# Performance work log

Hardware: AMD Instinct MI355X
Metric: run time of the kernel (lower is better)

The kernel has to match this reference:

```python
import jax, jax.numpy as jnp
import numpy as np

B, C, L = 32, 64, 4096
HIDDEN = 64
SR = 50.0
KS = (7, 15, 31, 63)
PHYS = 12
EPS_BN = 1e-5
EPS_GN = 1e-5


def _dwconv(x, w):
    # x: (B,C,L), w: (C,1,k) depthwise kernel, SAME padding for odd k
    k = w.shape[-1]
    p = (k - 1) // 2
    return jax.lax.conv_general_dilated(
        x, w, window_strides=(1,), padding=[(p, p)],
        dimension_numbers=('NCH', 'OIH', 'NCH'),
        feature_group_count=x.shape[1])


def _physics(x):
    b, c, l = x.shape
    svm = jnp.sqrt((x * x).sum(axis=1))                      # (B,L) channel norm
    svm_max = svm.max(axis=-1)
    svm_mean = svm.mean(axis=-1)
    svm_std = jnp.std(svm, axis=-1, ddof=1) + 1e-6           # torch.std is unbiased
    jerk = jnp.diff(x, axis=-1) * SR                         # (B,C,L-1)
    jerk_max = jnp.abs(jerk).max(axis=-1).mean(axis=-1)      # (B,)
    jerk_rate = jnp.diff(jerk, axis=-1) * SR
    jerk_rate_max = jnp.abs(jerk_rate).max(axis=-1).mean(axis=-1)
    sign_changes = (x[:, :, :-1] * x[:, :, 1:] < 0).astype(x.dtype)
    zcr = sign_changes.sum(axis=-1).mean(axis=-1) / l
    thr = (svm_mean + 2.0 * svm_std)[:, None]
    impact_duration = (svm > thr).astype(x.dtype).sum(axis=-1) / l
    hthr = (svm_mean + 3.0 * svm_std)[:, None]
    impact_ratio = (svm > hthr).astype(x.dtype).sum(axis=-1) / l
    free_fall = (svm < (svm_mean - svm_std)[:, None]).astype(x.dtype).sum(axis=-1) / l
    second_half = svm[:, l // 2:]
    post_stillness = jnp.tanh(1.0 / (jnp.std(second_half, axis=-1, ddof=1) + 1e-6))
    third = max(1, l // 3)
    pre_mean = svm[:, :third].mean(axis=-1)
    impact_peak = svm[:, third:2 * third].max(axis=-1)
    post_mean = svm[:, 2 * third:].mean(axis=-1)
    fall_phase = jax.nn.relu(impact_peak - pre_mean) + jax.nn.relu(impact_peak - post_mean)
    fall_phase = fall_phase / (jnp.abs(impact_peak) + 1e-6)
    spectrum = jnp.fft.rfft(x.astype(jnp.float32), axis=-1, norm='ortho')
    power = (jnp.abs(spectrum) ** 2).sum(axis=1)             # (B, L//2+1)
    freqs = jnp.linspace(0.0, 1.0, power.shape[-1], dtype=power.dtype)
    total_power = power.sum(axis=-1) + 1e-6
    spectral_centroid = (power * freqs).sum(axis=-1) / total_power
    high_freq_ratio = jnp.where(freqs > 0.4, power, 0.0).sum(axis=-1) / total_power
    feats = jnp.stack([svm_max, svm_mean, jerk_max, jerk_rate_max, zcr,
                       impact_duration, impact_ratio, post_stillness, free_fall,
                       spectral_centroid, high_freq_ratio, fall_phase], axis=-1)
    return jnp.nan_to_num(feats, nan=0.0, posinf=0.0, neginf=0.0).astype(x.dtype)


def _forward(x, dw_w7, dw_w15, dw_w31, dw_w63, bn_g, bn_b, bn_m, bn_v,
             comp_w1, comp_b1, comp_w2, comp_b2,
             pn_g, pn_b, pn_m, pn_v,
             pe_w1, pe_b1, pe_w2, pe_b2, pg_w, pg_b,
             temperature, gn_g, gn_b, proj_w, proj_b, res_scale):
    # 4 depthwise conv + BN(eval) branches
    branches = []
    for i, w in enumerate((dw_w7, dw_w15, dw_w31, dw_w63)):
        y = _dwconv(x, w)
        y = (y - bn_m[i][None, :, None]) / jnp.sqrt(bn_v[i][None, :, None] + EPS_BN) \
            * bn_g[i][None, :, None] + bn_b[i][None, :, None]
        branches.append(y)
    stacked = jnp.stack(branches, axis=1)                    # (B,4,C,L)
    # complexity net: global avg pool -> MLP
    xm = x.mean(axis=-1)                                     # (B,C)
    h = jax.nn.relu(xm @ comp_w1 + comp_b1)
    complexity_logits = h @ comp_w2 + comp_b2                # (B,4)
    # physics gate
    pf = _physics(x)                                         # (B,12)
    pf = (pf - pn_m) / jnp.sqrt(pn_v + EPS_BN) * pn_g + pn_b
    pe = jax.nn.relu(jax.nn.relu(pf @ pe_w1 + pe_b1) @ pe_w2 + pe_b2)
    physics_weights = jax.nn.sigmoid(pe @ pg_w + pg_b)       # (B,4)
    temp = jnp.maximum(temperature, 0.1)
    weights = jax.nn.softmax(complexity_logits * physics_weights / temp, axis=-1)
    mixed = jnp.einsum('bkcl,bk->bcl', stacked, weights)
    # proj: GroupNorm(1,C) -> GELU(exact) -> 1x1 conv
    mu = mixed.mean(axis=(1, 2), keepdims=True)
    var = mixed.var(axis=(1, 2), keepdims=True)
    gn = (mixed - mu) / jnp.sqrt(var + EPS_GN) * gn_g[None, :, None] + gn_b[None, :, None]
    act = jax.nn.gelu(gn, approximate=False)
    out = jnp.einsum('oc,bcl->bol', proj_w, act) + proj_b[None, :, None]
    return x + res_scale * out


def setup_inputs() -> dict:
    ks = jax.random.split(jax.random.key(0), 16)
    f32 = jnp.float32
    inp = {}
    inp['x'] = jax.random.normal(ks[0], (B, C, L), dtype=f32)
    for i, k in enumerate(KS):
        inp[f'dw_w{k}'] = jax.random.normal(ks[1 + i], (C, 1, k), dtype=f32) / np.sqrt(k)
    inp['bn_g'] = jnp.ones((4, C), f32)
    inp['bn_b'] = jnp.zeros((4, C), f32)
    inp['bn_m'] = 0.1 * jax.random.normal(ks[5], (4, C), dtype=f32)
    inp['bn_v'] = jax.random.uniform(ks[6], (4, C), dtype=f32, minval=0.5, maxval=1.5)
    inp['comp_w1'] = jax.random.normal(ks[7], (C, HIDDEN), dtype=f32) / np.sqrt(C)
    inp['comp_b1'] = jnp.zeros((HIDDEN,), f32)
    inp['comp_w2'] = jax.random.normal(ks[8], (HIDDEN, 4), dtype=f32) / np.sqrt(HIDDEN)
    inp['comp_b2'] = jnp.zeros((4,), f32)
    inp['pn_g'] = jnp.ones((PHYS,), f32)
    inp['pn_b'] = jnp.zeros((PHYS,), f32)
    inp['pn_m'] = 0.1 * jax.random.normal(ks[9], (PHYS,), dtype=f32)
    inp['pn_v'] = jax.random.uniform(ks[10], (PHYS,), dtype=f32, minval=0.5, maxval=1.5)
    inp['pe_w1'] = jax.random.normal(ks[11], (PHYS, 32), dtype=f32) / np.sqrt(PHYS)
    inp['pe_b1'] = jnp.zeros((32,), f32)
    inp['pe_w2'] = jax.random.normal(ks[12], (32, 32), dtype=f32) / np.sqrt(32)
    inp['pe_b2'] = jnp.zeros((32,), f32)
    inp['pg_w'] = jax.random.normal(ks[13], (32, 4), dtype=f32) / np.sqrt(32)
    inp['pg_b'] = jnp.zeros((4,), f32)
    inp['temperature'] = jnp.asarray(1.0, f32)
    inp['gn_g'] = jnp.ones((C,), f32)
    inp['gn_b'] = jnp.zeros((C,), f32)
    inp['proj_w'] = jax.random.normal(ks[14], (C, C), dtype=f32) / np.sqrt(C)
    inp['proj_b'] = jnp.zeros((C,), f32)
    inp['res_scale'] = jnp.asarray(0.5, f32)  # init is 0.0; 0.5 gives a non-trivial output
    return inp


def reference(x, dw_w7, dw_w15, dw_w31, dw_w63, bn_g, bn_b, bn_m, bn_v,
              comp_w1, comp_b1, comp_w2, comp_b2,
              pn_g, pn_b, pn_m, pn_v,
              pe_w1, pe_b1, pe_w2, pe_b2, pg_w, pg_b,
              temperature, gn_g, gn_b, proj_w, proj_b, res_scale):
    return _forward(x, dw_w7, dw_w15, dw_w31, dw_w63, bn_g, bn_b, bn_m, bn_v,
                    comp_w1, comp_b1, comp_w2, comp_b2, pn_g, pn_b, pn_m, pn_v,
                    pe_w1, pe_b1, pe_w2, pe_b2, pg_w, pg_b,
                    temperature, gn_g, gn_b, proj_w, proj_b, res_scale)
```

## Files before the change

### kernel.cpp

```cpp
#include <hip/hip_runtime.h>
#include <math.h>

#define LN 4096
#define CN 64
#define BQ 32
#define NTH 256

#define OFF_CHAN_SUM    0
#define OFF_CHAN_JERK   2048
#define OFF_CHAN_JRATE  4096
#define OFF_CHAN_ZCR    6144
#define OFF_SVMST_PART  8192
#define OFF_SPEC_PART   12288
#define OFF_EFF_B       15360
#define OFF_GNP         17408
#define OFF_EFF_W       21504
#define OFF_SVMBUF      152576

#define FP(i) ((i) + ((i) >> 4))

__device__ __forceinline__ void bfly4(float2& a, float2& b, float2& c, float2& d,
                                      float w1r, float w1i, float w2r, float w2i,
                                      float w3r, float w3i) {
  float t1r = b.x*w1r - b.y*w1i, t1i = b.x*w1i + b.y*w1r;
  float t2r = c.x*w2r - c.y*w2i, t2i = c.x*w2i + c.y*w2r;
  float t3r = d.x*w3r - d.y*w3i, t3i = d.x*w3i + d.y*w3r;
  float ar = a.x + t2r, ai = a.y + t2i;
  float br = a.x - t2r, bi = a.y - t2i;
  float cr = t1r + t3r, ci = t1i + t3i;
  float dr = t1r - t3r, di = t1i - t3i;
  a = make_float2(ar + cr, ai + ci);
  b = make_float2(br + di, bi - dr);
  c = make_float2(ar - cr, ai - ci);
  d = make_float2(br - di, bi + dr);
}

__global__ __launch_bounds__(NTH) void kS(const float* __restrict__ x, float* __restrict__ ws) {
  __shared__ __align__(16) char smraw[34880];
  int role = blockIdx.x;
  int t = threadIdx.x;

  if (role < 2048) {
    int bc = role;
    const float* row = x + (size_t)bc * LN;
    int l0 = t * 16;
    float rd[18];
    const float4* r4 = (const float4*)(row + l0);
#pragma unroll
    for (int q = 0; q < 4; q++) {
      float4 v = r4[q];
      rd[4*q] = v.x; rd[4*q+1] = v.y; rd[4*q+2] = v.z; rd[4*q+3] = v.w;
    }
    if (t < 255) { rd[16] = row[l0 + 16]; rd[17] = row[l0 + 17]; }
    else { rd[16] = 0.f; rd[17] = 0.f; }
    float lsum = 0.f, jm = 0.f, jrm = 0.f; int zc = 0;
#pragma unroll
    for (int i = 0; i < 16; i++) {
      float a = rd[i], b2 = rd[i+1];
      lsum += a;
      int l = l0 + i;
      if (l < LN - 1) {
        jm = fmaxf(jm, fabsf(b2 - a));
        zc += (a * b2 < 0.f);
        if (l < LN - 2) jrm = fmaxf(jrm, fabsf(rd[i+2] - 2.f*b2 + a));
      }
    }
    for (int off = 32; off > 0; off >>= 1) {
      lsum += __shfl_down(lsum, off);
      jm = fmaxf(jm, __shfl_down(jm, off));
      jrm = fmaxf(jrm, __shfl_down(jrm, off));
      zc += __shfl_down(zc, off);
    }
    float* s1 = (float*)smraw; float* s2_ = s1 + 4; float* s3 = s1 + 8; int* s4 = (int*)(s1 + 12);
    int w = t >> 6;
    if ((t & 63) == 0) { s1[w] = lsum; s2_[w] = jm; s3[w] = jrm; s4[w] = zc; }
    __syncthreads();
    if (t == 0) {
      float S = 0, J = 0, JR = 0; int Z = 0;
      for (int i = 0; i < 4; i++) { S += s1[i]; J = fmaxf(J, s2_[i]); JR = fmaxf(JR, s3[i]); Z += s4[i]; }
      ws[OFF_CHAN_SUM + bc]   = S;
      ws[OFF_CHAN_JERK + bc]  = J * 50.f;
      ws[OFF_CHAN_JRATE + bc] = JR * 2500.f;
      ws[OFF_CHAN_ZCR + bc]   = (float)Z;
    }
  } else if (role < 2560) {
    int blk = role - 2048;
    int b = blk >> 4, lt = blk & 15;
    int l = lt * 256 + t;
    const float* xb = x + (size_t)b * CN * LN + l;
    float acc = 0.f;
#pragma unroll
    for (int c = 0; c < CN; c++) { float v = xb[(size_t)c * LN]; acc = fmaf(v, v, acc); }
    float svm = sqrtf(acc);
    ws[OFF_SVMBUF + (size_t)b * LN + l] = svm;
    const int third = LN / 3;
    float vS = svm, vS2 = svm * svm;
    float vS2H  = (l >= LN/2) ? svm : 0.f;
    float vS2H2 = (l >= LN/2) ? svm * svm : 0.f;
    float vPRE  = (l < third) ? svm : 0.f;
    float vPOST = (l >= 2*third) ? svm : 0.f;
    float vMX = svm;
    float vMID = (l >= third && l < 2*third) ? svm : 0.f;
    for (int off = 32; off > 0; off >>= 1) {
      vS += __shfl_down(vS, off); vS2 += __shfl_down(vS2, off);
      vS2H += __shfl_down(vS2H, off); vS2H2 += __shfl_down(vS2H2, off);
      vPRE += __shfl_down(vPRE, off); vPOST += __shfl_down(vPOST, off);
      vMX = fmaxf(vMX, __shfl_down(vMX, off));
      vMID = fmaxf(vMID, __shfl_down(vMID, off));
    }
    float (*red)[4] = (float(*)[4])smraw;
    int w = t >> 6;
    if ((t & 63) == 0) {
      red[0][w] = vS; red[1][w] = vS2; red[2][w] = vMX; red[3][w] = vS2H;
      red[4][w] = vS2H2; red[5][w] = vPRE; red[6][w] = vMID; red[7][w] = vPOST;
    }
    __syncthreads();
    if (t == 0) {
      float* sp = ws + OFF_SVMST_PART + (size_t)blk * 8;
      sp[0] = red[0][0]+red[0][1]+red[0][2]+red[0][3];
      sp[1] = red[1][0]+red[1][1]+red[1][2]+red[1][3];
      sp[2] = fmaxf(fmaxf(red[2][0],red[2][1]),fmaxf(red[2][2],red[2][3]));
      sp[3] = red[3][0]+red[3][1]+red[3][2]+red[3][3];
      sp[4] = red[4][0]+red[4][1]+red[4][2]+red[4][3];
      sp[5] = red[5][0]+red[5][1]+red[5][2]+red[5][3];
      sp[6] = fmaxf(fmaxf(red[6][0],red[6][1]),fmaxf(red[6][2],red[6][3]));
      sp[7] = red[7][0]+red[7][1]+red[7][2]+red[7][3];
    }
  } else {
    int blk = role - 2560;
    int b = blk >> 5, cp = blk & 31;
    const float* r0 = x + ((size_t)b * CN + 2 * cp) * LN;
    const float* r1 = r0 + LN;
    float2* z = (float2*)smraw;
    float (*red)[4] = (float(*)[4])(smraw + 34816);
#pragma unroll
    for (int k = 0; k < 4; k++) {
      int n4 = (k * 256 + t) * 4;
      float4 a = *(const float4*)(r0 + n4);
      float4 c = *(const float4*)(r1 + n4);
      float ar[4] = {a.x, a.y, a.z, a.w}, cr[4] = {c.x, c.y, c.z, c.w};
#pragma unroll
      for (int q = 0; q < 4; q++) {
        unsigned n = (unsigned)(n4 + q);
        unsigned br = __brev(n) >> 20;
        unsigned dr = ((br & 0x555u) << 1) | ((br & 0xAAAu) >> 1);
        z[FP(dr)] = make_float2(ar[q], cr[q]);
      }
    }
    __syncthreads();
    const float c8r[4] = { 1.f, 0.92387953251f, 0.70710678119f, 0.38268343236f };
    const float c8i[4] = { 0.f, -0.38268343236f, -0.70710678119f, -0.92387953251f };
#pragma unroll
    for (int p = 0; p < 3; p++) {
      const int H = (p == 0) ? 1 : (p == 1) ? 16 : 256;
      int r = t & (H - 1);
      int B = ((t / H) * 16 * H) + r;
      float2 E[16];
#pragma unroll
      for (int q = 0; q < 16; q++) E[q] = z[FP(B + q * H)];
      float su, cu;
      sincospif((float)r / (8.0f * (float)H), &su, &cu);
      float ur = cu, ui = -su;
      float u2r = ur*ur - ui*ui, u2i = 2.f*ur*ui;
      float w1r = u2r*u2r - u2i*u2i, w1i = 2.f*u2r*u2i;
      float w2r = w1r*w1r - w1i*w1i, w2i = 2.f*w1r*w1i;
      float w3r = w2r*w1r - w2i*w1i, w3i = w2r*w1i + w2i*w1r;
#pragma unroll
      for (int m = 0; m < 4; m++)
        bfly4(E[4*m], E[4*m+1], E[4*m+2], E[4*m+3], w1r, w1i, w2r, w2i, w3r, w3i);
#pragma unroll
      for (int m = 0; m < 4; m++) {
        float W1r = ur*c8r[m] - ui*c8i[m];
        float W1i = ur*c8i[m] + ui*c8r[m];
        float W2r = W1r*W1r - W1i*W1i, W2i = 2.f*W1r*W1i;
        float W3r = W2r*W1r - W2i*W1i, W3i = W2r*W1i + W2i*W1r;
        bfly4(E[m], E[m+4], E[m+8], E[m+12], W1r, W1i, W2r, W2i, W3r, W3i);
      }
#pragma unroll
      for (int q = 0; q < 16; q++) z[FP(B + q * H)] = E[q];
      __syncthreads();
    }
    float tot = 0.f, cen = 0.f, hi = 0.f;
    for (int k = t; k <= LN / 2; k += NTH) {
      float p;
      if (k == 0 || k == LN / 2) {
        float2 v = z[FP(k)];
        p = v.x * v.x + v.y * v.y;
      } else {
        float2 zk = z[FP(k)], zn = z[FP(LN - k)];
        float a1 = zk.x + zn.x, a2 = zk.y - zn.y, a3 = zk.y + zn.y, a4 = zk.x - zn.x;
        p = 0.25f * (a1*a1 + a2*a2 + a3*a3 + a4*a4);
      }
      p *= (1.0f / LN);
      tot += p;
      cen += p * ((float)k * (1.0f / (LN / 2)));
      if (k >= 820) hi += p;
    }
    for (int off = 32; off > 0; off >>= 1) {
      tot += __shfl_down(tot, off);
      cen += __shfl_down(cen, off);
      hi  += __shfl_down(hi, off);
    }
    int w = t >> 6;
    if ((t & 63) == 0) { red[0][w] = tot; red[1][w] = cen; red[2][w] = hi; }
    __syncthreads();
    if (t == 0) {
      float* sp = ws + OFF_SPEC_PART + (size_t)blk * 3;
      sp[0] = red[0][0]+red[0][1]+red[0][2]+red[0][3];
      sp[1] = red[1][0]+red[1][1]+red[1][2]+red[1][3];
      sp[2] = red[2][0]+red[2][1]+red[2][2]+red[2][3];
    }
  }
}

__global__ __launch_bounds__(NTH) void k4_gate(
    const float* __restrict__ dw7, const float* __restrict__ dw15,
    const float* __restrict__ dw31, const float* __restrict__ dw63,
    const float* __restrict__ bn_g, const float* __restrict__ bn_b,
    const float* __restrict__ bn_m, const float* __restrict__ bn_v,
    const float* __restrict__ comp_w1, const float* __restrict__ comp_b1,
    const float* __restrict__ comp_w2, const float* __restrict__ comp_b2,
    const float* __restrict__ pn_g, const float* __restrict__ pn_b,
    const float* __restrict__ pn_m, const float* __restrict__ pn_v,
    const float* __restrict__ pe_w1, const float* __restrict__ pe_b1,
    const float* __restrict__ pe_w2, const float* __restrict__ pe_b2,
    const float* __restrict__ pg_w, const float* __restrict__ pg_b,
    const float* __restrict__ temperature,
    float* __restrict__ ws)
{
  int b = blockIdx.x, t = threadIdx.x;
  __shared__ float sp8[16][8];
  __shared__ float sp3[32][3];
  __shared__ float stv[10];
  __shared__ float bc2[2];
  __shared__ float xm[64], h[64], pf[12], pe1v[32], pe2v[32], lgts[4], wts[4];
  __shared__ int ri[3][4], cnts[3];
  if (t < 16) {
    const float* p = ws + OFF_SVMST_PART + (size_t)(b * 16 + t) * 8;
#pragma unroll
    for (int i = 0; i < 8; i++) sp8[t][i] = p[i];
  }
  if (t >= 32 && t < 64) {
    int i = t - 32;
    const float* p = ws + OFF_SPEC_PART + (size_t)(b * 32 + i) * 3;
    sp3[i][0] = p[0]; sp3[i][1] = p[1]; sp3[i][2] = p[2];
  }
  __syncthreads();
  if (t == 0) {
    float S=0,S2=0,MX=-1e30f,S2H=0,S2H2=0,PRE=0,MID=-1e30f,POST=0;
    for (int i = 0; i < 16; i++) {
      S += sp8[i][0]; S2 += sp8[i][1]; MX = fmaxf(MX, sp8[i][2]);
      S2H += sp8[i][3]; S2H2 += sp8[i][4]; PRE += sp8[i][5];
      MID = fmaxf(MID, sp8[i][6]); POST += sp8[i][7];
    }
    float tot=0,cen=0,hi=0;
    for (int i = 0; i < 32; i++) { tot += sp3[i][0]; cen += sp3[i][1]; hi += sp3[i][2]; }
    stv[0]=S; stv[1]=S2; stv[2]=MX; stv[3]=S2H; stv[4]=S2H2;
    stv[5]=PRE; stv[6]=MID; stv[7]=POST; stv[8]=cen/(tot+1e-6f); stv[9]=hi/(tot+1e-6f);
    float mean = S * (1.f / LN);
    float var = (S2 - S * S * (1.f / LN)) * (1.f / (LN - 1));
    var = fmaxf(var, 0.f);
    bc2[0] = mean;
    bc2[1] = sqrtf(var) + 1e-6f;
  }
  __syncthreads();
  float mean = bc2[0], stde = bc2[1];
  float thr2 = mean + 2.f * stde, thr3 = mean + 3.f * stde, thrf = mean - stde;
  const float* svm = ws + OFF_SVMBUF + (size_t)b * LN;
  int c2 = 0, c3 = 0, cf = 0;
  for (int l = t; l < LN; l += NTH) {
    float v = svm[l];
    c2 += (v > thr2); c3 += (v > thr3); cf += (v < thrf);
  }
  for (int off = 32; off > 0; off >>= 1) {
    c2 += __shfl_down(c2, off); c3 += __shfl_down(c3, off); cf += __shfl_down(cf, off);
  }
  int w = t >> 6;
  if ((t & 63) == 0) { ri[0][w] = c2; ri[1][w] = c3; ri[2][w] = cf; }
  float j = 0.f, jr = 0.f, zz = 0.f;
  if (t < 64) {
    xm[t] = ws[OFF_CHAN_SUM + b * 64 + t] * (1.0f / LN);
    j  = ws[OFF_CHAN_JERK + b * 64 + t];
    jr = ws[OFF_CHAN_JRATE + b * 64 + t];
    zz = ws[OFF_CHAN_ZCR + b * 64 + t];
    for (int off = 32; off > 0; off >>= 1) {
      j += __shfl_down(j, off); jr += __shfl_down(jr, off); zz += __shfl_down(zz, off);
    }
  }
  __syncthreads();
  if (t == 0) {
    cnts[0] = ri[0][0]+ri[0][1]+ri[0][2]+ri[0][3];
    cnts[1] = ri[1][0]+ri[1][1]+ri[1][2]+ri[1][3];
    cnts[2] = ri[2][0]+ri[2][1]+ri[2][2]+ri[2][3];
    const int third = LN / 3;
    float S2H = stv[3], S2H2 = stv[4];
    float n2 = (float)(LN / 2);
    float var2 = (S2H2 - S2H * S2H / n2) / (n2 - 1.f);
    var2 = fmaxf(var2, 0.f);
    float post_still = tanhf(1.f / (sqrtf(var2) + 1e-6f));
    float pre_mean = stv[5] / (float)third;
    float post_mean = stv[7] / (float)(LN - 2 * third);
    float pk = stv[6];
    float fp = fmaxf(pk - pre_mean, 0.f) + fmaxf(pk - post_mean, 0.f);
    fp = fp / (fabsf(pk) + 1e-6f);
    pf[0] = stv[2];
    pf[1] = mean;
    pf[2] = j * (1.f / 64);
    pf[3] = jr * (1.f / 64);
    pf[4] = (zz * (1.f / 64)) * (1.f / LN);
    pf[5] = (float)cnts[0] / LN;
    pf[6] = (float)cnts[1] / LN;
    pf[7] = post_still;
    pf[8] = (float)cnts[2] / LN;
    pf[9] = stv[8];
    pf[10] = stv[9];
    pf[11] = fp;
  }
  __syncthreads();
  if (t < 12) pf[t] = (pf[t] - pn_m[t]) * rsqrtf(pn_v[t] + 1e-5f) * pn_g[t] + pn_b[t];
  __syncthreads();
  if (t < 64) {
    float hv = comp_b1[t];
    for (int i = 0; i < 64; i++) hv = fmaf(xm[i], comp_w1[i * 64 + t], hv);
    h[t] = fmaxf(hv, 0.f);
  }
  if (t < 32) {
    float v = pe_b1[t];
    for (int i = 0; i < 12; i++) v = fmaf(pf[i], pe_w1[i * 32 + t], v);
    pe1v[t] = fmaxf(v, 0.f);
  }
  __syncthreads();
  if (t < 32) {
    float v = pe_b2[t];
    for (int i = 0; i < 32; i++) v = fmaf(pe1v[i], pe_w2[i * 32 + t], v);
    pe2v[t] = fmaxf(v, 0.f);
  }
  __syncthreads();
  if (t < 4) {
    float v = comp_b2[t];
    for (int i = 0; i < 64; i++) v = fmaf(h[i], comp_w2[i * 4 + t], v);
    float g = pg_b[t];
    for (int i = 0; i < 32; i++) g = fmaf(pe2v[i], pg_w[i * 4 + t], g);
    g = 1.f / (1.f + expf(-g));
    float temp = fmaxf(temperature[0], 0.1f);
    lgts[t] = v * g / temp;
  }
  __syncthreads();
  if (t < 4) {
    float m = fmaxf(fmaxf(lgts[0], lgts[1]), fmaxf(lgts[2], lgts[3]));
    float den = expf(lgts[0]-m) + expf(lgts[1]-m) + expf(lgts[2]-m) + expf(lgts[3]-m);
    wts[t] = expf(lgts[t] - m) / den;
  }
  __syncthreads();
  if (t < 64) {
    int c = t;
    float w0 = wts[0], w1 = wts[1], w2 = wts[2], w3 = wts[3];
    float sc0 = bn_g[0*64+c] * rsqrtf(bn_v[0*64+c] + 1e-5f);
    float sc1 = bn_g[1*64+c] * rsqrtf(bn_v[1*64+c] + 1e-5f);
    float sc2 = bn_g[2*64+c] * rsqrtf(bn_v[2*64+c] + 1e-5f);
    float sc3 = bn_g[3*64+c] * rsqrtf(bn_v[3*64+c] + 1e-5f);
    float o0 = bn_b[0*64+c] - bn_m[0*64+c] * sc0;
    float o1 = bn_b[1*64+c] - bn_m[1*64+c] * sc1;
    float o2 = bn_b[2*64+c] - bn_m[2*64+c] * sc2;
    float o3 = bn_b[3*64+c] - bn_m[3*64+c] * sc3;
    ws[OFF_EFF_B + b * 64 + c] = w0*o0 + w1*o1 + w2*o2 + w3*o3;
    float a0 = w0*sc0, a1 = w1*sc1, a2 = w2*sc2, a3 = w3*sc3;
    float* eff = ws + OFF_EFF_W + (size_t)(b * 64 + c) * 64;
    for (int tau = 0; tau < 64; tau++) {
      float v = 0.f;
      if (tau < 63) {
        v = a3 * dw63[c * 63 + tau];
        int i7 = tau - 28;  if (i7 >= 0 && i7 < 7)   v = fmaf(a0, dw7[c * 7 + i7], v);
        int i15 = tau - 24; if (i15 >= 0 && i15 < 15) v = fmaf(a1, dw15[c * 15 + i15], v);
        int i31 = tau - 16; if (i31 >= 0 && i31 < 31) v = fmaf(a2, dw31[c * 31 + i31], v);
      }
      eff[tau] = v;
    }
  }
}

__device__ __forceinline__ float4 ldmask(const float* __restrict__ row, int idx) {
  int idxc = idx < 0 ? 0 : (idx > LN - 4 ? LN - 4 : idx);
  float4 v = *(const float4*)(row + idxc);
  float m = (idx == idxc) ? 1.f : 0.f;
  v.x *= m; v.y *= m; v.z *= m; v.w *= m;
  return v;
}

#define F16(wv,a0,a1,a2,a3,a4,a5,a6,a7,a8,a9,aA,aB,aC,aD,aE,aF) \
  acc[0]=fmaf(wv,a0,acc[0]);  acc[1]=fmaf(wv,a1,acc[1]);  acc[2]=fmaf(wv,a2,acc[2]);  acc[3]=fmaf(wv,a3,acc[3]);  \
  acc[4]=fmaf(wv,a4,acc[4]);  acc[5]=fmaf(wv,a5,acc[5]);  acc[6]=fmaf(wv,a6,acc[6]);  acc[7]=fmaf(wv,a7,acc[7]);  \
  acc[8]=fmaf(wv,a8,acc[8]);  acc[9]=fmaf(wv,a9,acc[9]);  acc[10]=fmaf(wv,aA,acc[10]); acc[11]=fmaf(wv,aB,acc[11]); \
  acc[12]=fmaf(wv,aC,acc[12]); acc[13]=fmaf(wv,aD,acc[13]); acc[14]=fmaf(wv,aE,acc[14]); acc[15]=fmaf(wv,aF,acc[15]);

__global__ __launch_bounds__(NTH) void k5_conv(const float* __restrict__ x,
                                               float* __restrict__ ws,
                                               float* __restrict__ mixed_out) {
  int bc = blockIdx.x;
  int t = threadIdx.x;
  __shared__ float wt[64];
  __shared__ float biasS;
  __shared__ double rda[2][4];
  if (t < 64) wt[t] = ws[OFF_EFF_W + (size_t)bc * 64 + t];
  if (t == 0) biasS = ws[OFF_EFF_B + bc];
  const float* row = x + (size_t)bc * LN;
  int l0 = t * 16;
  int g0 = l0 - 32;
  float4 R0 = ldmask(row, g0);
  float4 R1 = ldmask(row, g0 + 4);
  float4 R2 = ldmask(row, g0 + 8);
  float4 R3 = ldmask(row, g0 + 12);
  float4 R4 = ldmask(row, g0 + 16);
  __syncthreads();
  float bias = biasS;
  float acc[16];
#pragma unroll
  for (int jj = 0; jj < 16; jj++) acc[jj] = bias;
#pragma unroll
  for (int g = 0; g < 16; g++) {
    float w0 = wt[4*g], w1 = wt[4*g+1], w2 = wt[4*g+2], w3 = wt[4*g+3];
    F16(w0, R0.y,R0.z,R0.w,R1.x,R1.y,R1.z,R1.w,R2.x,R2.y,R2.z,R2.w,R3.x,R3.y,R3.z,R3.w,R4.x)
    F16(w1, R0.z,R0.w,R1.x,R1.y,R1.z,R1.w,R2.x,R2.y,R2.z,R2.w,R3.x,R3.y,R3.z,R3.w,R4.x,R4.y)
    F16(w2, R0.w,R1.x,R1.y,R1.z,R1.w,R2.x,R2.y,R2.z,R2.w,R3.x,R3.y,R3.z,R3.w,R4.x,R4.y,R4.z)
    F16(w3, R1.x,R1.y,R1.z,R1.w,R2.x,R2.y,R2.z,R2.w,R3.x,R3.y,R3.z,R3.w,R4.x,R4.y,R4.z,R4.w)
    if (g < 15) {
      R0 = R1; R1 = R2; R2 = R3; R3 = R4;
      R4 = ldmask(row, g0 + 4 * (g + 5));
    }
  }
  double ls = 0, ls2 = 0;
#pragma unroll
  for (int jj = 0; jj < 16; jj++) { float v = acc[jj]; ls += v; ls2 += (double)v * (double)v; }
  for (int off = 32; off > 0; off >>= 1) {
    ls += __shfl_down(ls, off);
    ls2 += __shfl_down(ls2, off);
  }
  int w = t >> 6;
  if ((t & 63) == 0) { rda[0][w] = ls; rda[1][w] = ls2; }
  __syncthreads();
  if (t == 0) {
    double* gp = (double*)(ws + OFF_GNP);
    gp[2 * bc + 0] = rda[0][0]+rda[0][1]+rda[0][2]+rda[0][3];
    gp[2 * bc + 1] = rda[1][0]+rda[1][1]+rda[1][2]+rda[1][3];
  }
  float* dst = mixed_out + (size_t)bc * LN + l0;
#pragma unroll
  for (int q = 0; q < 4; q++) {
    float4 v; v.x = acc[4*q]; v.y = acc[4*q+1]; v.z = acc[4*q+2]; v.w = acc[4*q+3];
    *(float4*)(dst + 4 * q) = v;
  }
}

__global__ __launch_bounds__(NTH) void k6_final(const float* __restrict__ x,
    const float* __restrict__ proj_w, const float* __restrict__ proj_b,
    const float* __restrict__ gn_g, const float* __restrict__ gn_b,
    const float* __restrict__ res_scale,
    const float* __restrict__ ws, float* out) {
  int blk = blockIdx.x;
  int b = blk >> 5;
  int l0 = (blk & 31) * 128;
  __shared__ float actS[64 * 128];
  __shared__ float Wt[64 * 64];
  __shared__ double rg[2][4];
  __shared__ float bcst[2];
  int t = threadIdx.x;
  {
    const double* gp = (const double*)(ws + OFF_GNP) + (size_t)b * CN * 2;
    double s1 = 0, s2 = 0;
    for (int i = t; i < CN; i += NTH) { s1 += gp[2*i]; s2 += gp[2*i+1]; }
    for (int off = 32; off > 0; off >>= 1) { s1 += __shfl_down(s1, off); s2 += __shfl_down(s2, off); }
    int w = t >> 6;
    if ((t & 63) == 0) { rg[0][w] = s1; rg[1][w] = s2; }
    __syncthreads();
    if (t == 0) {
      double S1 = rg[0][0]+rg[0][1]+rg[0][2]+rg[0][3];
      double S2 = rg[1][0]+rg[1][1]+rg[1][2]+rg[1][3];
      const double NN = 64.0 * 4096.0;
      double mud = S1 / NN;
      bcst[0] = (float)mud;
      bcst[1] = rsqrtf((float)(S2 / NN - mud * mud) + 1e-5f);
    }
  }
  for (int i = t; i < 4096; i += NTH) {
    int o = i & 63, c = i >> 6;
    Wt[c * 64 + o] = proj_w[o * 64 + c];
  }
  __syncthreads();
  float mu = bcst[0], rstd = bcst[1];
  const float* mx = out + (size_t)b * CN * LN;
  for (int i = t; i < 8192; i += NTH) {
    int c = i >> 7, l = i & 127;
    float v = mx[(size_t)c * LN + l0 + l];
    float g = (v - mu) * rstd * gn_g[c] + gn_b[c];
    float a = 0.5f * g * (1.f + erff(g * 0.70710678118654752f));
    actS[c * 128 + l] = a;
  }
  __syncthreads();
  int lg = t & 31;
  int og = (t >> 5) * 8;
  float4 acc4[8];
#pragma unroll
  for (int q = 0; q < 8; q++) { acc4[q].x = 0.f; acc4[q].y = 0.f; acc4[q].z = 0.f; acc4[q].w = 0.f; }
  for (int c = 0; c < 64; c++) {
    float4 a = *(const float4*)&actS[c * 128 + lg * 4];
    float4 wlo = *(const float4*)&Wt[c * 64 + og];
    float4 whi = *(const float4*)&Wt[c * 64 + og + 4];
    float wv[8] = { wlo.x, wlo.y, wlo.z, wlo.w, whi.x, whi.y, whi.z, whi.w };
#pragma unroll
    for (int q = 0; q < 8; q++) {
      acc4[q].x = fmaf(wv[q], a.x, acc4[q].x);
      acc4[q].y = fmaf(wv[q], a.y, acc4[q].y);
      acc4[q].z = fmaf(wv[q], a.z, acc4[q].z);
      acc4[q].w = fmaf(wv[q], a.w, acc4[q].w);
    }
  }
  float rsv = res_scale[0];
  const float* xb = x + (size_t)b * CN * LN;
  float* ob = out + (size_t)b * CN * LN;
#pragma unroll
  for (int q = 0; q < 8; q++) {
    int o = og + q;
    float pb = proj_b[o];
    size_t base = (size_t)o * LN + l0 + lg * 4;
    float4 xv = *(const float4*)&xb[base];
    float4 r;
    r.x = xv.x + rsv * (acc4[q].x + pb);
    r.y = xv.y + rsv * (acc4[q].y + pb);
    r.z = xv.z + rsv * (acc4[q].z + pb);
    r.w = xv.w + rsv * (acc4[q].w + pb);
    *(float4*)&ob[base] = r;
  }
}

extern "C" void kernel_launch(void* const* d_in, const int* in_sizes, int n_in,
                              void* d_out, int out_size, void* d_ws, size_t ws_size,
                              hipStream_t stream) {
  const float* x        = (const float*)d_in[0];
  const float* dw7      = (const float*)d_in[1];
  const float* dw15     = (const float*)d_in[2];
  const float* dw31     = (const float*)d_in[3];
  const float* dw63     = (const float*)d_in[4];
  const float* bn_g     = (const float*)d_in[5];
  const float* bn_b     = (const float*)d_in[6];
  const float* bn_m     = (const float*)d_in[7];
  const float* bn_v     = (const float*)d_in[8];
  const float* comp_w1  = (const float*)d_in[9];
  const float* comp_b1  = (const float*)d_in[10];
  const float* comp_w2  = (const float*)d_in[11];
  const float* comp_b2  = (const float*)d_in[12];
  const float* pn_g     = (const float*)d_in[13];
  const float* pn_b     = (const float*)d_in[14];
  const float* pn_m     = (const float*)d_in[15];
  const float* pn_v     = (const float*)d_in[16];
  const float* pe_w1    = (const float*)d_in[17];
  const float* pe_b1    = (const float*)d_in[18];
  const float* pe_w2    = (const float*)d_in[19];
  const float* pe_b2    = (const float*)d_in[20];
  const float* pg_w     = (const float*)d_in[21];
  const float* pg_b     = (const float*)d_in[22];
  const float* temperature = (const float*)d_in[23];
  const float* gn_g     = (const float*)d_in[24];
  const float* gn_b     = (const float*)d_in[25];
  const float* proj_w   = (const float*)d_in[26];
  const float* proj_b   = (const float*)d_in[27];
  const float* res_scale= (const float*)d_in[28];
  float* ws = (float*)d_ws;
  float* out = (float*)d_out;

  hipLaunchKernelGGL(kS, dim3(2048 + 512 + 1024), dim3(NTH), 0, stream, x, ws);
  hipLaunchKernelGGL(k4_gate, dim3(BQ), dim3(NTH), 0, stream,
                     dw7, dw15, dw31, dw63, bn_g, bn_b, bn_m, bn_v,
                     comp_w1, comp_b1, comp_w2, comp_b2,
                     pn_g, pn_b, pn_m, pn_v, pe_w1, pe_b1, pe_w2, pe_b2,
                     pg_w, pg_b, temperature, ws);
  hipLaunchKernelGGL(k5_conv, dim3(BQ * CN), dim3(NTH), 0, stream, x, ws, out);
  hipLaunchKernelGGL(k6_final, dim3(BQ * 32), dim3(NTH), 0, stream,
                     x, proj_w, proj_b, gn_g, gn_b, res_scale, ws, out);
}
```

Baseline: 235.0 us.

## Fuse stats passes into FFT blocks and merge gate computation into conv kernel

The per-channel jerk/zero-crossing stats and the SVM partial sums are folded into the FFT blocks, so one 1024-block kernel reads x once for all three instead of running separate role groups. The per-batch gate kernel is merged into the depthwise conv kernel, with each block recomputing the gate redundantly, which drops a launch and the effective-weight workspace round-trip. The final projection kernel is retiled to process two 64-column halves with smaller shared memory, aiming for higher occupancy. The cost is duplicated gate arithmetic in every conv block and more work per FFT block.

New measurement: 228.7 us. -2.7%, faster.

```diff
diff --git a/kernel.cpp b/kernel.cpp
--- a/kernel.cpp
+++ b/kernel.cpp
@@ -3,7 +3,6 @@
 
 #define LN 4096
 #define CN 64
-#define BQ 32
 #define NTH 256
 
 #define OFF_CHAN_SUM    0
@@ -11,11 +10,9 @@
 #define OFF_CHAN_JRATE  4096
 #define OFF_CHAN_ZCR    6144
 #define OFF_SVMST_PART  8192
-#define OFF_SPEC_PART   12288
-#define OFF_EFF_B       15360
-#define OFF_GNP         17408
-#define OFF_EFF_W       21504
-#define OFF_SVMBUF      152576
+#define OFF_SPEC_PART   16384
+#define OFF_GNP         19584
+#define OFF_SVMBUF      27776
 
 #define FP(i) ((i) + ((i) >> 4))
 
@@ -35,131 +32,164 @@
   d = make_float2(br - di, bi + dr);
 }
 
-__global__ __launch_bounds__(NTH) void kS(const float* __restrict__ x, float* __restrict__ ws) {
-  __shared__ __align__(16) char smraw[34880];
-  int role = blockIdx.x;
+__device__ __forceinline__ float4 ldmask(const float* __restrict__ row, int idx) {
+  int idxc = idx < 0 ? 0 : (idx > LN - 4 ? LN - 4 : idx);
+  float4 v = *(const float4*)(row + idxc);
+  float m = (idx == idxc) ? 1.f : 0.f;
+  v.x *= m; v.y *= m; v.z *= m; v.w *= m;
+  return v;
+}
+
+#define F16(wv,a0,a1,a2,a3,a4,a5,a6,a7,a8,a9,aA,aB,aC,aD,aE,aF) \
+  acc[0]=fmaf(wv,a0,acc[0]);  acc[1]=fmaf(wv,a1,acc[1]);  acc[2]=fmaf(wv,a2,acc[2]);  acc[3]=fmaf(wv,a3,acc[3]);  \
+  acc[4]=fmaf(wv,a4,acc[4]);  acc[5]=fmaf(wv,a5,acc[5]);  acc[6]=fmaf(wv,a6,acc[6]);  acc[7]=fmaf(wv,a7,acc[7]);  \
+  acc[8]=fmaf(wv,a8,acc[8]);  acc[9]=fmaf(wv,a9,acc[9]);  acc[10]=fmaf(wv,aA,acc[10]); acc[11]=fmaf(wv,aB,acc[11]); \
+  acc[12]=fmaf(wv,aC,acc[12]); acc[13]=fmaf(wv,aD,acc[13]); acc[14]=fmaf(wv,aE,acc[14]); acc[15]=fmaf(wv,aF,acc[15]);
+
+__global__ __launch_bounds__(NTH) void k1_spec(const float* __restrict__ x, float* __restrict__ ws) {
+  __shared__ __align__(16) char smraw[35072];
+  int i = blockIdx.x;
+  int b = i >> 5, sl = i & 31;
   int t = threadIdx.x;
 
-  if (role < 2048) {
-    int bc = role;
-    const float* row = x + (size_t)bc * LN;
-    int l0 = t * 16;
-    float rd[18];
-    const float4* r4 = (const float4*)(row + l0);
-#pragma unroll
-    for (int q = 0; q < 4; q++) {
-      float4 v = r4[q];
-      rd[4*q] = v.x; rd[4*q+1] = v.y; rd[4*q+2] = v.z; rd[4*q+3] = v.w;
-    }
-    if (t < 255) { rd[16] = row[l0 + 16]; rd[17] = row[l0 + 17]; }
-    else { rd[16] = 0.f; rd[17] = 0.f; }
-    float lsum = 0.f, jm = 0.f, jrm = 0.f; int zc = 0;
-#pragma unroll
-    for (int i = 0; i < 16; i++) {
-      float a = rd[i], b2 = rd[i+1];
-      lsum += a;
-      int l = l0 + i;
-      if (l < LN - 1) {
-        jm = fmaxf(jm, fabsf(b2 - a));
-        zc += (a * b2 < 0.f);
-        if (l < LN - 2) jrm = fmaxf(jrm, fabsf(rd[i+2] - 2.f*b2 + a));
-      }
-    }
-    for (int off = 32; off > 0; off >>= 1) {
-      lsum += __shfl_down(lsum, off);
-      jm = fmaxf(jm, __shfl_down(jm, off));
-      jrm = fmaxf(jrm, __shfl_down(jrm, off));
-      zc += __shfl_down(zc, off);
-    }
-    float* s1 = (float*)smraw; float* s2_ = s1 + 4; float* s3 = s1 + 8; int* s4 = (int*)(s1 + 12);
-    int w = t >> 6;
-    if ((t & 63) == 0) { s1[w] = lsum; s2_[w] = jm; s3[w] = jrm; s4[w] = zc; }
-    __syncthreads();
-    if (t == 0) {
-      float S = 0, J = 0, JR = 0; int Z = 0;
-      for (int i = 0; i < 4; i++) { S += s1[i]; J = fmaxf(J, s2_[i]); JR = fmaxf(JR, s3[i]); Z += s4[i]; }
-      ws[OFF_CHAN_SUM + bc]   = S;
-      ws[OFF_CHAN_JERK + bc]  = J * 50.f;
-      ws[OFF_CHAN_JRATE + bc] = JR * 2500.f;
-      ws[OFF_CHAN_ZCR + bc]   = (float)Z;
-    }
-  } else if (role < 2560) {
-    int blk = role - 2048;
-    int b = blk >> 4, lt = blk & 15;
-    int l = lt * 256 + t;
+  {
+    float* tmp = (float*)smraw;
+    float (*sred)[8] = (float(*)[8])(smraw + 512);
+    int lt = t & 127, ch = t >> 7;
+    int l = sl * 128 + lt;
     const float* xb = x + (size_t)b * CN * LN + l;
     float acc = 0.f;
 #pragma unroll
-    for (int c = 0; c < CN; c++) { float v = xb[(size_t)c * LN]; acc = fmaf(v, v, acc); }
-    float svm = sqrtf(acc);
-    ws[OFF_SVMBUF + (size_t)b * LN + l] = svm;
-    const int third = LN / 3;
-    float vS = svm, vS2 = svm * svm;
-    float vS2H  = (l >= LN/2) ? svm : 0.f;
-    float vS2H2 = (l >= LN/2) ? svm * svm : 0.f;
-    float vPRE  = (l < third) ? svm : 0.f;
-    float vPOST = (l >= 2*third) ? svm : 0.f;
-    float vMX = svm;
-    float vMID = (l >= third && l < 2*third) ? svm : 0.f;
-    for (int off = 32; off > 0; off >>= 1) {
-      vS += __shfl_down(vS, off); vS2 += __shfl_down(vS2, off);
-      vS2H += __shfl_down(vS2H, off); vS2H2 += __shfl_down(vS2H2, off);
-      vPRE += __shfl_down(vPRE, off); vPOST += __shfl_down(vPOST, off);
-      vMX = fmaxf(vMX, __shfl_down(vMX, off));
-      vMID = fmaxf(vMID, __shfl_down(vMID, off));
-    }
-    float (*red)[4] = (float(*)[4])smraw;
-    int w = t >> 6;
-    if ((t & 63) == 0) {
-      red[0][w] = vS; red[1][w] = vS2; red[2][w] = vMX; red[3][w] = vS2H;
-      red[4][w] = vS2H2; red[5][w] = vPRE; red[6][w] = vMID; red[7][w] = vPOST;
+    for (int cc = 0; cc < 32; cc++) {
+      float v = xb[(size_t)(ch * 32 + cc) * LN];
+      acc = fmaf(v, v, acc);
+    }
+    if (ch == 1) tmp[lt] = acc;
+    __syncthreads();
+    if (ch == 0) {
+      acc += tmp[lt];
+      float svm = sqrtf(acc);
+      ws[OFF_SVMBUF + (size_t)b * LN + l] = svm;
+      const int third = LN / 3;
+      float vS = svm, vS2 = svm * svm;
+      float vS2H  = (l >= LN/2) ? svm : 0.f;
+      float vS2H2 = (l >= LN/2) ? svm * svm : 0.f;
+      float vPRE  = (l < third) ? svm : 0.f;
+      float vPOST = (l >= 2*third) ? svm : 0.f;
+      float vMX = svm;
+      float vMID = (l >= third && l < 2*third) ? svm : 0.f;
+      for (int off = 32; off > 0; off >>= 1) {
+        vS += __shfl_down(vS, off); vS2 += __shfl_down(vS2, off);
+        vS2H += __shfl_down(vS2H, off); vS2H2 += __shfl_down(vS2H2, off);
+        vPRE += __shfl_down(vPRE, off); vPOST += __shfl_down(vPOST, off);
+        vMX = fmaxf(vMX, __shfl_down(vMX, off));
+        vMID = fmaxf(vMID, __shfl_down(vMID, off));
+      }
+      if ((t & 63) == 0) {
+        int w = t >> 6;
+        sred[w][0]=vS; sred[w][1]=vS2; sred[w][2]=vMX; sred[w][3]=vS2H;
+        sred[w][4]=vS2H2; sred[w][5]=vPRE; sred[w][6]=vMID; sred[w][7]=vPOST;
+      }
     }
     __syncthreads();
     if (t == 0) {
-      float* sp = ws + OFF_SVMST_PART + (size_t)blk * 8;
-      sp[0] = red[0][0]+red[0][1]+red[0][2]+red[0][3];
-      sp[1] = red[1][0]+red[1][1]+red[1][2]+red[1][3];
-      sp[2] = fmaxf(fmaxf(red[2][0],red[2][1]),fmaxf(red[2][2],red[2][3]));
-      sp[3] = red[3][0]+red[3][1]+red[3][2]+red[3][3];
-      sp[4] = red[4][0]+red[4][1]+red[4][2]+red[4][3];
-      sp[5] = red[5][0]+red[5][1]+red[5][2]+red[5][3];
-      sp[6] = fmaxf(fmaxf(red[6][0],red[6][1]),fmaxf(red[6][2],red[6][3]));
-      sp[7] = red[7][0]+red[7][1]+red[7][2]+red[7][3];
-    }
-  } else {
-    int blk = role - 2560;
-    int b = blk >> 5, cp = blk & 31;
-    const float* r0 = x + ((size_t)b * CN + 2 * cp) * LN;
+      float* sp = ws + OFF_SVMST_PART + (size_t)(b * 32 + sl) * 8;
+      sp[0]=sred[0][0]+sred[1][0];
+      sp[1]=sred[0][1]+sred[1][1];
+      sp[2]=fmaxf(sred[0][2],sred[1][2]);
+      sp[3]=sred[0][3]+sred[1][3];
+      sp[4]=sred[0][4]+sred[1][4];
+      sp[5]=sred[0][5]+sred[1][5];
+      sp[6]=fmaxf(sred[0][6],sred[1][6]);
+      sp[7]=sred[0][7]+sred[1][7];
+    }
+    __syncthreads();
+  }
+
+  {
+    const float* r0 = x + ((size_t)b * CN + 2 * sl) * LN;
     const float* r1 = r0 + LN;
     float2* z = (float2*)smraw;
-    float (*red)[4] = (float(*)[4])(smraw + 34816);
+    float (*sred8)[8] = (float(*)[8])(smraw + 34816);
+    float s0 = 0.f, jm0 = 0.f, jr0 = 0.f; int zc0 = 0;
+    float s1v = 0.f, jm1 = 0.f, jr1 = 0.f; int zc1 = 0;
 #pragma unroll
     for (int k = 0; k < 4; k++) {
       int n4 = (k * 256 + t) * 4;
       float4 a = *(const float4*)(r0 + n4);
       float4 c = *(const float4*)(r1 + n4);
-      float ar[4] = {a.x, a.y, a.z, a.w}, cr[4] = {c.x, c.y, c.z, c.w};
+      float a4 = __shfl_down(a.x, 1), a5 = __shfl_down(a.y, 1);
+      float c4 = __shfl_down(c.x, 1), c5 = __shfl_down(c.y, 1);
+      if ((t & 63) == 63) {
+        a4 = (n4 + 4 < LN) ? r0[n4 + 4] : 0.f;
+        a5 = (n4 + 5 < LN) ? r0[n4 + 5] : 0.f;
+        c4 = (n4 + 4 < LN) ? r1[n4 + 4] : 0.f;
+        c5 = (n4 + 5 < LN) ? r1[n4 + 5] : 0.f;
+      }
+      bool nl = (n4 + 4 < LN);
+      s0 += a.x + a.y + a.z + a.w;
+      jm0 = fmaxf(jm0, fmaxf(fmaxf(fabsf(a.y-a.x), fabsf(a.z-a.y)), fabsf(a.w-a.z)));
+      zc0 += (a.x*a.y < 0.f) + (a.y*a.z < 0.f) + (a.z*a.w < 0.f);
+      jr0 = fmaxf(jr0, fmaxf(fabsf(a.z - 2.f*a.y + a.x), fabsf(a.w - 2.f*a.z + a.y)));
+      if (nl) {
+        jm0 = fmaxf(jm0, fabsf(a4 - a.w));
+        zc0 += (a.w * a4 < 0.f);
+        jr0 = fmaxf(jr0, fmaxf(fabsf(a4 - 2.f*a.w + a.z), fabsf(a5 - 2.f*a4 + a.w)));
+      }
+      s1v += c.x + c.y + c.z + c.w;
+      jm1 = fmaxf(jm1, fmaxf(fmaxf(fabsf(c.y-c.x), fabsf(c.z-c.y)), fabsf(c.w-c.z)));
+      zc1 += (c.x*c.y < 0.f) + (c.y*c.z < 0.f) + (c.z*c.w < 0.f);
+      jr1 = fmaxf(jr1, fmaxf(fabsf(c.z - 2.f*c.y + c.x), fabsf(c.w - 2.f*c.z + c.y)));
+      if (nl) {
+        jm1 = fmaxf(jm1, fabsf(c4 - c.w));
+        zc1 += (c.w * c4 < 0.f);
+        jr1 = fmaxf(jr1, fmaxf(fabsf(c4 - 2.f*c.w + c.z), fabsf(c5 - 2.f*c4 + c.w)));
+      }
+      float ar[4] = {a.x, a.y, a.z, a.w}, crr[4] = {c.x, c.y, c.z, c.w};
 #pragma unroll
       for (int q = 0; q < 4; q++) {
         unsigned n = (unsigned)(n4 + q);
         unsigned br = __brev(n) >> 20;
         unsigned dr = ((br & 0x555u) << 1) | ((br & 0xAAAu) >> 1);
-        z[FP(dr)] = make_float2(ar[q], cr[q]);
-      }
-    }
-    __syncthreads();
+        z[FP(dr)] = make_float2(ar[q], crr[q]);
+      }
+    }
+    for (int off = 32; off > 0; off >>= 1) {
+      s0 += __shfl_down(s0, off); jm0 = fmaxf(jm0, __shfl_down(jm0, off));
+      jr0 = fmaxf(jr0, __shfl_down(jr0, off)); zc0 += __shfl_down(zc0, off);
+      s1v += __shfl_down(s1v, off); jm1 = fmaxf(jm1, __shfl_down(jm1, off));
+      jr1 = fmaxf(jr1, __shfl_down(jr1, off)); zc1 += __shfl_down(zc1, off);
+    }
+    if ((t & 63) == 0) {
+      int w = t >> 6;
+      sred8[w][0]=s0; sred8[w][1]=jm0; sred8[w][2]=jr0; sred8[w][3]=(float)zc0;
+      sred8[w][4]=s1v; sred8[w][5]=jm1; sred8[w][6]=jr1; sred8[w][7]=(float)zc1;
+    }
+    __syncthreads();
+    if (t == 0) {
+      int bc0 = b * CN + 2 * sl;
+      float S0=0,J0=0,JR0=0,Z0=0,S1=0,J1=0,JR1=0,Z1=0;
+      for (int w = 0; w < 4; w++) {
+        S0 += sred8[w][0]; J0 = fmaxf(J0, sred8[w][1]); JR0 = fmaxf(JR0, sred8[w][2]); Z0 += sred8[w][3];
+        S1 += sred8[w][4]; J1 = fmaxf(J1, sred8[w][5]); JR1 = fmaxf(JR1, sred8[w][6]); Z1 += sred8[w][7];
+      }
+      ws[OFF_CHAN_SUM + bc0]       = S0;           ws[OFF_CHAN_SUM + bc0 + 1]   = S1;
+      ws[OFF_CHAN_JERK + bc0]      = J0 * 50.f;    ws[OFF_CHAN_JERK + bc0 + 1]  = J1 * 50.f;
+      ws[OFF_CHAN_JRATE + bc0]     = JR0 * 2500.f; ws[OFF_CHAN_JRATE + bc0 + 1] = JR1 * 2500.f;
+      ws[OFF_CHAN_ZCR + bc0]       = Z0;           ws[OFF_CHAN_ZCR + bc0 + 1]   = Z1;
+    }
     const float c8r[4] = { 1.f, 0.92387953251f, 0.70710678119f, 0.38268343236f };
     const float c8i[4] = { 0.f, -0.38268343236f, -0.70710678119f, -0.92387953251f };
 #pragma unroll
     for (int p = 0; p < 3; p++) {
       const int H = (p == 0) ? 1 : (p == 1) ? 16 : 256;
-      int r = t & (H - 1);
-      int B = ((t / H) * 16 * H) + r;
+      int rr = t & (H - 1);
+      int B = ((t / H) * 16 * H) + rr;
       float2 E[16];
 #pragma unroll
       for (int q = 0; q < 16; q++) E[q] = z[FP(B + q * H)];
       float su, cu;
-      sincospif((float)r / (8.0f * (float)H), &su, &cu);
+      sincospif((float)rr / (8.0f * (float)H), &su, &cu);
       float ur = cu, ui = -su;
       float u2r = ur*ur - ui*ui, u2i = 2.f*ur*ui;
       float w1r = u2r*u2r - u2i*u2i, w1i = 2.f*u2r*u2i;
@@ -188,8 +218,8 @@
         p = v.x * v.x + v.y * v.y;
       } else {
         float2 zk = z[FP(k)], zn = z[FP(LN - k)];
-        float a1 = zk.x + zn.x, a2 = zk.y - zn.y, a3 = zk.y + zn.y, a4 = zk.x - zn.x;
-        p = 0.25f * (a1*a1 + a2*a2 + a3*a3 + a4*a4);
+        float a1 = zk.x + zn.x, a2 = zk.y - zn.y, a3 = zk.y + zn.y, a4v = zk.x - zn.x;
+        p = 0.25f * (a1*a1 + a2*a2 + a3*a3 + a4v*a4v);
       }
       p *= (1.0f / LN);
       tot += p;
@@ -201,19 +231,20 @@
       cen += __shfl_down(cen, off);
       hi  += __shfl_down(hi, off);
     }
-    int w = t >> 6;
-    if ((t & 63) == 0) { red[0][w] = tot; red[1][w] = cen; red[2][w] = hi; }
+    float (*redS)[4] = (float(*)[4])(smraw + 34816);
+    if ((t & 63) == 0) { int w = t >> 6; redS[0][w] = tot; redS[1][w] = cen; redS[2][w] = hi; }
     __syncthreads();
     if (t == 0) {
-      float* sp = ws + OFF_SPEC_PART + (size_t)blk * 3;
-      sp[0] = red[0][0]+red[0][1]+red[0][2]+red[0][3];
-      sp[1] = red[1][0]+red[1][1]+red[1][2]+red[1][3];
-      sp[2] = red[2][0]+red[2][1]+red[2][2]+red[2][3];
+      float* sp = ws + OFF_SPEC_PART + (size_t)(b * 32 + sl) * 3;
+      sp[0] = redS[0][0]+redS[0][1]+redS[0][2]+redS[0][3];
+      sp[1] = redS[1][0]+redS[1][1]+redS[1][2]+redS[1][3];
+      sp[2] = redS[2][0]+redS[2][1]+redS[2][2]+redS[2][3];
     }
   }
 }
 
-__global__ __launch_bounds__(NTH) void k4_gate(
+__global__ __launch_bounds__(NTH) void k2_conv(
+    const float* __restrict__ x,
     const float* __restrict__ dw7, const float* __restrict__ dw15,
     const float* __restrict__ dw31, const float* __restrict__ dw63,
     const float* __restrict__ bn_g, const float* __restrict__ bn_b,
@@ -226,37 +257,43 @@
     const float* __restrict__ pe_w2, const float* __restrict__ pe_b2,
     const float* __restrict__ pg_w, const float* __restrict__ pg_b,
     const float* __restrict__ temperature,
-    float* __restrict__ ws)
+    float* __restrict__ ws, float* __restrict__ out)
 {
-  int b = blockIdx.x, t = threadIdx.x;
-  __shared__ float sp8[16][8];
+  int i = blockIdx.x;
+  int b = i >> 5, sl = i & 31;
+  int t = threadIdx.x;
+  __shared__ float sp8[32][8];
   __shared__ float sp3[32][3];
   __shared__ float stv[10];
   __shared__ float bc2[2];
-  __shared__ float xm[64], h[64], pf[12], pe1v[32], pe2v[32], lgts[4], wts[4];
+  __shared__ float xm[64], h[64], pf[12], pe1v[32], pe2v[32], lgts[4], swts[4];
   __shared__ int ri[3][4], cnts[3];
-  if (t < 16) {
-    const float* p = ws + OFF_SVMST_PART + (size_t)(b * 16 + t) * 8;
-#pragma unroll
-    for (int i = 0; i < 8; i++) sp8[t][i] = p[i];
+  __shared__ float cwt[2][64];
+  __shared__ float cbias[2];
+  __shared__ double rda[2][4];
+
+  if (t < 32) {
+    const float* p = ws + OFF_SVMST_PART + (size_t)(b * 32 + t) * 8;
+#pragma unroll
+    for (int q = 0; q < 8; q++) sp8[t][q] = p[q];
   }
   if (t >= 32 && t < 64) {
-    int i = t - 32;
-    const float* p = ws + OFF_SPEC_PART + (size_t)(b * 32 + i) * 3;
-    sp3[i][0] = p[0]; sp3[i][1] = p[1]; sp3[i][2] = p[2];
+    int q = t - 32;
+    const float* p = ws + OFF_SPEC_PART + (size_t)(b * 32 + q) * 3;
+    sp3[q][0] = p[0]; sp3[q][1] = p[1]; sp3[q][2] = p[2];
   }
   __syncthreads();
   if (t == 0) {
     float S=0,S2=0,MX=-1e30f,S2H=0,S2H2=0,PRE=0,MID=-1e30f,POST=0;
-    for (int i = 0; i < 16; i++) {
-      S += sp8[i][0]; S2 += sp8[i][1]; MX = fmaxf(MX, sp8[i][2]);
-      S2H += sp8[i][3]; S2H2 += sp8[i][4]; PRE += sp8[i][5];
-      MID = fmaxf(MID, sp8[i][6]); POST += sp8[i][7];
-    }
-    float tot=0,cen=0,hi=0;
-    for (int i = 0; i < 32; i++) { tot += sp3[i][0]; cen += sp3[i][1]; hi += sp3[i][2]; }
+    for (int q = 0; q < 32; q++) {
+      S += sp8[q][0]; S2 += sp8[q][1]; MX = fmaxf(MX, sp8[q][2]);
+      S2H += sp8[q][3]; S2H2 += sp8[q][4]; PRE += sp8[q][5];
+      MID = fmaxf(MID, sp8[q][6]); POST += sp8[q][7];
+    }
+    float tt=0,ce=0,hh=0;
+    for (int q = 0; q < 32; q++) { tt += sp3[q][0]; ce += sp3[q][1]; hh += sp3[q][2]; }
     stv[0]=S; stv[1]=S2; stv[2]=MX; stv[3]=S2H; stv[4]=S2H2;
-    stv[5]=PRE; stv[6]=MID; stv[7]=POST; stv[8]=cen/(tot+1e-6f); stv[9]=hi/(tot+1e-6f);
+    stv[5]=PRE; stv[6]=MID; stv[7]=POST; stv[8]=ce/(tt+1e-6f); stv[9]=hh/(tt+1e-6f);
     float mean = S * (1.f / LN);
     float var = (S2 - S * S * (1.f / LN)) * (1.f / (LN - 1));
     var = fmaxf(var, 0.f);
@@ -267,16 +304,18 @@
   float mean = bc2[0], stde = bc2[1];
   float thr2 = mean + 2.f * stde, thr3 = mean + 3.f * stde, thrf = mean - stde;
   const float* svm = ws + OFF_SVMBUF + (size_t)b * LN;
-  int c2 = 0, c3 = 0, cf = 0;
+  int cc2 = 0, cc3 = 0, ccf = 0;
   for (int l = t; l < LN; l += NTH) {
     float v = svm[l];
-    c2 += (v > thr2); c3 += (v > thr3); cf += (v < thrf);
+    cc2 += (v > thr2); cc3 += (v > thr3); ccf += (v < thrf);
   }
   for (int off = 32; off > 0; off >>= 1) {
-    c2 += __shfl_down(c2, off); c3 += __shfl_down(c3, off); cf += __shfl_down(cf, off);
-  }
-  int w = t >> 6;
-  if ((t & 63) == 0) { ri[0][w] = c2; ri[1][w] = c3; ri[2][w] = cf; }
+    cc2 += __shfl_down(cc2, off); cc3 += __shfl_down(cc3, off); ccf += __shfl_down(ccf, off);
+  }
+  {
+    int w = t >> 6;
+    if ((t & 63) == 0) { ri[0][w] = cc2; ri[1][w] = cc3; ri[2][w] = ccf; }
+  }
   float j = 0.f, jr = 0.f, zz = 0.f;
   if (t < 64) {
     xm[t] = ws[OFF_CHAN_SUM + b * 64 + t] * (1.0f / LN);
@@ -301,8 +340,8 @@
     float pre_mean = stv[5] / (float)third;
     float post_mean = stv[7] / (float)(LN - 2 * third);
     float pk = stv[6];
-    float fp = fmaxf(pk - pre_mean, 0.f) + fmaxf(pk - post_mean, 0.f);
-    fp = fp / (fabsf(pk) + 1e-6f);
+    float fp2 = fmaxf(pk - pre_mean, 0.f) + fmaxf(pk - post_mean, 0.f);
+    fp2 = fp2 / (fabsf(pk) + 1e-6f);
     pf[0] = stv[2];
     pf[1] = mean;
     pf[2] = j * (1.f / 64);
@@ -314,33 +353,33 @@
     pf[8] = (float)cnts[2] / LN;
     pf[9] = stv[8];
     pf[10] = stv[9];
-    pf[11] = fp;
+    pf[11] = fp2;
   }
   __syncthreads();
   if (t < 12) pf[t] = (pf[t] - pn_m[t]) * rsqrtf(pn_v[t] + 1e-5f) * pn_g[t] + pn_b[t];
   __syncthreads();
   if (t < 64) {
     float hv = comp_b1[t];
-    for (int i = 0; i < 64; i++) hv = fmaf(xm[i], comp_w1[i * 64 + t], hv);
+    for (int q = 0; q < 64; q++) hv = fmaf(xm[q], comp_w1[q * 64 + t], hv);
     h[t] = fmaxf(hv, 0.f);
   }
   if (t < 32) {
     float v = pe_b1[t];
-    for (int i = 0; i < 12; i++) v = fmaf(pf[i], pe_w1[i * 32 + t], v);
+    for (int q = 0; q < 12; q++) v = fmaf(pf[q], pe_w1[q * 32 + t], v);
     pe1v[t] = fmaxf(v, 0.f);
   }
   __syncthreads();
   if (t < 32) {
     float v = pe_b2[t];
-    for (int i = 0; i < 32; i++) v = fmaf(pe1v[i], pe_w2[i * 32 + t], v);
+    for (int q = 0; q < 32; q++) v = fmaf(pe1v[q], pe_w2[q * 32 + t], v);
     pe2v[t] = fmaxf(v, 0.f);
   }
   __syncthreads();
   if (t < 4) {
     float v = comp_b2[t];
-    for (int i = 0; i < 64; i++) v = fmaf(h[i], comp_w2[i * 4 + t], v);
+    for (int q = 0; q < 64; q++) v = fmaf(h[q], comp_w2[q * 4 + t], v);
     float g = pg_b[t];
-    for (int i = 0; i < 32; i++) g = fmaf(pe2v[i], pg_w[i * 4 + t], g);
+    for (int q = 0; q < 32; q++) g = fmaf(pe2v[q], pg_w[q * 4 + t], g);
     g = 1.f / (1.f + expf(-g));
     float temp = fmaxf(temperature[0], 0.1f);
     lgts[t] = v * g / temp;
@@ -349,186 +388,169 @@
   if (t < 4) {
     float m = fmaxf(fmaxf(lgts[0], lgts[1]), fmaxf(lgts[2], lgts[3]));
     float den = expf(lgts[0]-m) + expf(lgts[1]-m) + expf(lgts[2]-m) + expf(lgts[3]-m);
-    wts[t] = expf(lgts[t] - m) / den;
-  }
-  __syncthreads();
-  if (t < 64) {
-    int c = t;
-    float w0 = wts[0], w1 = wts[1], w2 = wts[2], w3 = wts[3];
+    swts[t] = expf(lgts[t] - m) / den;
+  }
+  __syncthreads();
+
+  if (t < 128) {
+    int rr = t >> 6, tau = t & 63;
+    int c = 2 * sl + rr;
+    float w0 = swts[0], w1 = swts[1], w2 = swts[2], w3 = swts[3];
     float sc0 = bn_g[0*64+c] * rsqrtf(bn_v[0*64+c] + 1e-5f);
     float sc1 = bn_g[1*64+c] * rsqrtf(bn_v[1*64+c] + 1e-5f);
     float sc2 = bn_g[2*64+c] * rsqrtf(bn_v[2*64+c] + 1e-5f);
     float sc3 = bn_g[3*64+c] * rsqrtf(bn_v[3*64+c] + 1e-5f);
-    float o0 = bn_b[0*64+c] - bn_m[0*64+c] * sc0;
-    float o1 = bn_b[1*64+c] - bn_m[1*64+c] * sc1;
-    float o2 = bn_b[2*64+c] - bn_m[2*64+c] * sc2;
-    float o3 = bn_b[3*64+c] - bn_m[3*64+c] * sc3;
-    ws[OFF_EFF_B + b * 64 + c] = w0*o0 + w1*o1 + w2*o2 + w3*o3;
     float a0 = w0*sc0, a1 = w1*sc1, a2 = w2*sc2, a3 = w3*sc3;
-    float* eff = ws + OFF_EFF_W + (size_t)(b * 64 + c) * 64;
-    for (int tau = 0; tau < 64; tau++) {
-      float v = 0.f;
-      if (tau < 63) {
-        v = a3 * dw63[c * 63 + tau];
-        int i7 = tau - 28;  if (i7 >= 0 && i7 < 7)   v = fmaf(a0, dw7[c * 7 + i7], v);
-        int i15 = tau - 24; if (i15 >= 0 && i15 < 15) v = fmaf(a1, dw15[c * 15 + i15], v);
-        int i31 = tau - 16; if (i31 >= 0 && i31 < 31) v = fmaf(a2, dw31[c * 31 + i31], v);
-      }
-      eff[tau] = v;
-    }
+    if (tau == 0) {
+      float o0 = bn_b[0*64+c] - bn_m[0*64+c] * sc0;
+      float o1 = bn_b[1*64+c] - bn_m[1*64+c] * sc1;
+      float o2 = bn_b[2*64+c] - bn_m[2*64+c] * sc2;
+      float o3 = bn_b[3*64+c] - bn_m[3*64+c] * sc3;
+      cbias[rr] = w0*o0 + w1*o1 + w2*o2 + w3*o3;
+    }
+    float v = 0.f;
+    if (tau < 63) {
+      v = a3 * dw63[c * 63 + tau];
+      int i7 = tau - 28;  if (i7 >= 0 && i7 < 7)    v = fmaf(a0, dw7[c * 7 + i7], v);
+      int i15 = tau - 24; if (i15 >= 0 && i15 < 15) v = fmaf(a1, dw15[c * 15 + i15], v);
+      int i31 = tau - 16; if (i31 >= 0 && i31 < 31) v = fmaf(a2, dw31[c * 31 + i31], v);
+    }
+    cwt[rr][tau] = v;
+  }
+  __syncthreads();
+
+#pragma unroll 1
+  for (int r = 0; r < 2; r++) {
+    int c = 2 * sl + r;
+    const float* row = x + ((size_t)b * CN + c) * LN;
+    const float* wtp = cwt[r];
+    float bias = cbias[r];
+    int l0 = t * 16, g0 = l0 - 32;
+    float4 R0 = ldmask(row, g0);
+    float4 R1 = ldmask(row, g0 + 4);
+    float4 R2 = ldmask(row, g0 + 8);
+    float4 R3 = ldmask(row, g0 + 12);
+    float4 R4 = ldmask(row, g0 + 16);
+    float acc[16];
+#pragma unroll
+    for (int jj = 0; jj < 16; jj++) acc[jj] = bias;
+#pragma unroll
+    for (int g = 0; g < 16; g++) {
+      float w0 = wtp[4*g], w1 = wtp[4*g+1], w2 = wtp[4*g+2], w3 = wtp[4*g+3];
+      F16(w0, R0.y,R0.z,R0.w,R1.x,R1.y,R1.z,R1.w,R2.x,R2.y,R2.z,R2.w,R3.x,R3.y,R3.z,R3.w,R4.x)
+      F16(w1, R0.z,R0.w,R1.x,R1.y,R1.z,R1.w,R2.x,R2.y,R2.z,R2.w,R3.x,R3.y,R3.z,R3.w,R4.x,R4.y)
+      F16(w2, R0.w,R1.x,R1.y,R1.z,R1.w,R2.x,R2.y,R2.z,R2.w,R3.x,R3.y,R3.z,R3.w,R4.x,R4.y,R4.z)
+      F16(w3, R1.x,R1.y,R1.z,R1.w,R2.x,R2.y,R2.z,R2.w,R3.x,R3.y,R3.z,R3.w,R4.x,R4.y,R4.z,R4.w)
+      if (g < 15) {
+        R0 = R1; R1 = R2; R2 = R3; R3 = R4;
+        R4 = ldmask(row, g0 + 4 * (g + 5));
+      }
+    }
+    double ls = 0, ls2 = 0;
+#pragma unroll
+    for (int jj = 0; jj < 16; jj++) { float v = acc[jj]; ls += v; ls2 += (double)v * (double)v; }
+    for (int off = 32; off > 0; off >>= 1) {
+      ls += __shfl_down(ls, off);
+      ls2 += __shfl_down(ls2, off);
+    }
+    int w = t >> 6;
+    if ((t & 63) == 0) { rda[0][w] = ls; rda[1][w] = ls2; }
+    float* dst = out + (size_t)(b * CN + c) * LN + l0;
+#pragma unroll
+    for (int q = 0; q < 4; q++) {
+      float4 v4; v4.x = acc[4*q]; v4.y = acc[4*q+1]; v4.z = acc[4*q+2]; v4.w = acc[4*q+3];
+      *(float4*)(dst + 4 * q) = v4;
+    }
+    __syncthreads();
+    if (t == 0) {
+      double* gp = (double*)(ws + OFF_GNP);
+      gp[2 * (b * CN + c) + 0] = rda[0][0]+rda[0][1]+rda[0][2]+rda[0][3];
+      gp[2 * (b * CN + c) + 1] = rda[1][0]+rda[1][1]+rda[1][2]+rda[1][3];
+    }
+    __syncthreads();
   }
 }
 
-__device__ __forceinline__ float4 ldmask(const float* __restrict__ row, int idx) {
-  int idxc = idx < 0 ? 0 : (idx > LN - 4 ? LN - 4 : idx);
-  float4 v = *(const float4*)(row + idxc);
-  float m = (idx == idxc) ? 1.f : 0.f;
-  v.x *= m; v.y *= m; v.z *= m; v.w *= m;
-  return v;
-}
-
-#define F16(wv,a0,a1,a2,a3,a4,a5,a6,a7,a8,a9,aA,aB,aC,aD,aE,aF) \
-  acc[0]=fmaf(wv,a0,acc[0]);  acc[1]=fmaf(wv,a1,acc[1]);  acc[2]=fmaf(wv,a2,acc[2]);  acc[3]=fmaf(wv,a3,acc[3]);  \
-  acc[4]=fmaf(wv,a4,acc[4]);  acc[5]=fmaf(wv,a5,acc[5]);  acc[6]=fmaf(wv,a6,acc[6]);  acc[7]=fmaf(wv,a7,acc[7]);  \
-  acc[8]=fmaf(wv,a8,acc[8]);  acc[9]=fmaf(wv,a9,acc[9]);  acc[10]=fmaf(wv,aA,acc[10]); acc[11]=fmaf(wv,aB,acc[11]); \
-  acc[12]=fmaf(wv,aC,acc[12]); acc[13]=fmaf(wv,aD,acc[13]); acc[14]=fmaf(wv,aE,acc[14]); acc[15]=fmaf(wv,aF,acc[15]);
-
-__global__ __launch_bounds__(NTH) void k5_conv(const float* __restrict__ x,
-                                               float* __restrict__ ws,
-                                               float* __restrict__ mixed_out) {
-  int bc = blockIdx.x;
-  int t = threadIdx.x;
-  __shared__ float wt[64];
-  __shared__ float biasS;
-  __shared__ double rda[2][4];
-  if (t < 64) wt[t] = ws[OFF_EFF_W + (size_t)bc * 64 + t];
-  if (t == 0) biasS = ws[OFF_EFF_B + bc];
-  const float* row = x + (size_t)bc * LN;
-  int l0 = t * 16;
-  int g0 = l0 - 32;
-  float4 R0 = ldmask(row, g0);
-  float4 R1 = ldmask(row, g0 + 4);
-  float4 R2 = ldmask(row, g0 + 8);
-  float4 R3 = ldmask(row, g0 + 12);
-  float4 R4 = ldmask(row, g0 + 16);
-  __syncthreads();
-  float bias = biasS;
-  float acc[16];
-#pragma unroll
-  for (int jj = 0; jj < 16; jj++) acc[jj] = bias;
-#pragma unroll
-  for (int g = 0; g < 16; g++) {
-    float w0 = wt[4*g], w1 = wt[4*g+1], w2 = wt[4*g+2], w3 = wt[4*g+3];
-    F16(w0, R0.y,R0.z,R0.w,R1.x,R1.y,R1.z,R1.w,R2.x,R2.y,R2.z,R2.w,R3.x,R3.y,R3.z,R3.w,R4.x)
-    F16(w1, R0.z,R0.w,R1.x,R1.y,R1.z,R1.w,R2.x,R2.y,R2.z,R2.w,R3.x,R3.y,R3.z,R3.w,R4.x,R4.y)
-    F16(w2, R0.w,R1.x,R1.y,R1.z,R1.w,R2.x,R2.y,R2.z,R2.w,R3.x,R3.y,R3.z,R3.w,R4.x,R4.y,R4.z)
-    F16(w3, R1.x,R1.y,R1.z,R1.w,R2.x,R2.y,R2.z,R2.w,R3.x,R3.y,R3.z,R3.w,R4.x,R4.y,R4.z,R4.w)
-    if (g < 15) {
-      R0 = R1; R1 = R2; R2 = R3; R3 = R4;
-      R4 = ldmask(row, g0 + 4 * (g + 5));
-    }
-  }
-  double ls = 0, ls2 = 0;
-#pragma unroll
-  for (int jj = 0; jj < 16; jj++) { float v = acc[jj]; ls += v; ls2 += (double)v * (double)v; }
-  for (int off = 32; off > 0; off >>= 1) {
-    ls += __shfl_down(ls, off);
-    ls2 += __shfl_down(ls2, off);
-  }
-  int w = t >> 6;
-  if ((t & 63) == 0) { rda[0][w] = ls; rda[1][w] = ls2; }
-  __syncthreads();
-  if (t == 0) {
-    double* gp = (double*)(ws + OFF_GNP);
-    gp[2 * bc + 0] = rda[0][0]+rda[0][1]+rda[0][2]+rda[0][3];
-    gp[2 * bc + 1] = rda[1][0]+rda[1][1]+rda[1][2]+rda[1][3];
-  }
-  float* dst = mixed_out + (size_t)bc * LN + l0;
-#pragma unroll
-  for (int q = 0; q < 4; q++) {
-    float4 v; v.x = acc[4*q]; v.y = acc[4*q+1]; v.z = acc[4*q+2]; v.w = acc[4*q+3];
-    *(float4*)(dst + 4 * q) = v;
-  }
-}
-
-__global__ __launch_bounds__(NTH) void k6_final(const float* __restrict__ x,
+__global__ __launch_bounds__(NTH) void k3_final(const float* __restrict__ x,
     const float* __restrict__ proj_w, const float* __restrict__ proj_b,
     const float* __restrict__ gn_g, const float* __restrict__ gn_b,
     const float* __restrict__ res_scale,
     const float* __restrict__ ws, float* out) {
-  int blk = blockIdx.x;
-  int b = blk >> 5;
-  int l0 = (blk & 31) * 128;
-  __shared__ float actS[64 * 128];
-  __shared__ float Wt[64 * 64];
-  __shared__ double rg[2][4];
-  __shared__ float bcst[2];
+  __shared__ __align__(16) char smraw[32840];
+  int i = blockIdx.x;
+  int b = i >> 5, sl = i & 31;
   int t = threadIdx.x;
+  float* Wt   = (float*)smraw;
+  float* actS = (float*)(smraw + 16384);
+  double (*rg)[4] = (double(*)[4])(smraw + 32768);
+  float* bcst = (float*)(smraw + 32832);
+  const double* gp = (const double*)(ws + OFF_GNP) + (size_t)b * CN * 2;
+  double g1 = 0, g2 = 0;
+  if (t < CN) { g1 = gp[2*t]; g2 = gp[2*t+1]; }
+  for (int off = 32; off > 0; off >>= 1) { g1 += __shfl_down(g1, off); g2 += __shfl_down(g2, off); }
   {
-    const double* gp = (const double*)(ws + OFF_GNP) + (size_t)b * CN * 2;
-    double s1 = 0, s2 = 0;
-    for (int i = t; i < CN; i += NTH) { s1 += gp[2*i]; s2 += gp[2*i+1]; }
-    for (int off = 32; off > 0; off >>= 1) { s1 += __shfl_down(s1, off); s2 += __shfl_down(s2, off); }
     int w = t >> 6;
-    if ((t & 63) == 0) { rg[0][w] = s1; rg[1][w] = s2; }
-    __syncthreads();
-    if (t == 0) {
-      double S1 = rg[0][0]+rg[0][1]+rg[0][2]+rg[0][3];
-      double S2 = rg[1][0]+rg[1][1]+rg[1][2]+rg[1][3];
-      const double NN = 64.0 * 4096.0;
-      double mud = S1 / NN;
-      bcst[0] = (float)mud;
-      bcst[1] = rsqrtf((float)(S2 / NN - mud * mud) + 1e-5f);
-    }
-  }
-  for (int i = t; i < 4096; i += NTH) {
-    int o = i & 63, c = i >> 6;
+    if ((t & 63) == 0) { rg[0][w] = g1; rg[1][w] = g2; }
+  }
+  for (int q = t; q < 4096; q += NTH) {
+    int o = q & 63, c = q >> 6;
     Wt[c * 64 + o] = proj_w[o * 64 + c];
   }
   __syncthreads();
+  if (t == 0) {
+    double S1 = rg[0][0]+rg[0][1]+rg[0][2]+rg[0][3];
+    double S2 = rg[1][0]+rg[1][1]+rg[1][2]+rg[1][3];
+    const double NN = 64.0 * 4096.0;
+    double mud = S1 / NN;
+    bcst[0] = (float)mud;
+    bcst[1] = rsqrtf((float)(S2 / NN - mud * mud) + 1e-5f);
+  }
+  __syncthreads();
   float mu = bcst[0], rstd = bcst[1];
+  float rsv = res_scale[0];
   const float* mx = out + (size_t)b * CN * LN;
-  for (int i = t; i < 8192; i += NTH) {
-    int c = i >> 7, l = i & 127;
-    float v = mx[(size_t)c * LN + l0 + l];
-    float g = (v - mu) * rstd * gn_g[c] + gn_b[c];
-    float a = 0.5f * g * (1.f + erff(g * 0.70710678118654752f));
-    actS[c * 128 + l] = a;
-  }
-  __syncthreads();
-  int lg = t & 31;
-  int og = (t >> 5) * 8;
-  float4 acc4[8];
-#pragma unroll
-  for (int q = 0; q < 8; q++) { acc4[q].x = 0.f; acc4[q].y = 0.f; acc4[q].z = 0.f; acc4[q].w = 0.f; }
-  for (int c = 0; c < 64; c++) {
-    float4 a = *(const float4*)&actS[c * 128 + lg * 4];
-    float4 wlo = *(const float4*)&Wt[c * 64 + og];
-    float4 whi = *(const float4*)&Wt[c * 64 + og + 4];
-    float wv[8] = { wlo.x, wlo.y, wlo.z, wlo.w, whi.x, whi.y, whi.z, whi.w };
-#pragma unroll
-    for (int q = 0; q < 8; q++) {
-      acc4[q].x = fmaf(wv[q], a.x, acc4[q].x);
-      acc4[q].y = fmaf(wv[q], a.y, acc4[q].y);
-      acc4[q].z = fmaf(wv[q], a.z, acc4[q].z);
-      acc4[q].w = fmaf(wv[q], a.w, acc4[q].w);
-    }
-  }
-  float rsv = res_scale[0];
   const float* xb = x + (size_t)b * CN * LN;
   float* ob = out + (size_t)b * CN * LN;
-#pragma unroll
-  for (int q = 0; q < 8; q++) {
-    int o = og + q;
-    float pb = proj_b[o];
-    size_t base = (size_t)o * LN + l0 + lg * 4;
-    float4 xv = *(const float4*)&xb[base];
-    float4 r;
-    r.x = xv.x + rsv * (acc4[q].x + pb);
-    r.y = xv.y + rsv * (acc4[q].y + pb);
-    r.z = xv.z + rsv * (acc4[q].z + pb);
-    r.w = xv.w + rsv * (acc4[q].w + pb);
-    *(float4*)&ob[base] = r;
+#pragma unroll 1
+  for (int hh = 0; hh < 2; hh++) {
+    int lbase = sl * 128 + hh * 64;
+    for (int q = t; q < 4096; q += NTH) {
+      int c = q >> 6, l = q & 63;
+      float v = mx[(size_t)c * LN + lbase + l];
+      float g = (v - mu) * rstd * gn_g[c] + gn_b[c];
+      actS[c * 64 + l] = 0.5f * g * (1.f + erff(g * 0.70710678118654752f));
+    }
+    __syncthreads();
+    int lq = t & 15, og = (t >> 4) * 4;
+    float4 acc4[4];
+#pragma unroll
+    for (int oo = 0; oo < 4; oo++) acc4[oo] = make_float4(0.f, 0.f, 0.f, 0.f);
+    for (int c = 0; c < 64; c++) {
+      float4 av = *(const float4*)&actS[c * 64 + lq * 4];
+      float4 wv = *(const float4*)&Wt[c * 64 + og];
+      float wsc[4] = {wv.x, wv.y, wv.z, wv.w};
+#pragma unroll
+      for (int oo = 0; oo < 4; oo++) {
+        acc4[oo].x = fmaf(wsc[oo], av.x, acc4[oo].x);
+        acc4[oo].y = fmaf(wsc[oo], av.y, acc4[oo].y);
+        acc4[oo].z = fmaf(wsc[oo], av.z, acc4[oo].z);
+        acc4[oo].w = fmaf(wsc[oo], av.w, acc4[oo].w);
+      }
+    }
+#pragma unroll
+    for (int oo = 0; oo < 4; oo++) {
+      int o = og + oo;
+      float pb = proj_b[o];
+      size_t base = (size_t)o * LN + lbase + lq * 4;
+      float4 xv = *(const float4*)&xb[base];
+      float4 rr2;
+      rr2.x = xv.x + rsv * (acc4[oo].x + pb);
+      rr2.y = xv.y + rsv * (acc4[oo].y + pb);
+      rr2.z = xv.z + rsv * (acc4[oo].z + pb);
+      rr2.w = xv.w + rsv * (acc4[oo].w + pb);
+      *(float4*)&ob[base] = rr2;
+    }
+    __syncthreads();
   }
 }
 
@@ -567,13 +589,12 @@
   float* ws = (float*)d_ws;
   float* out = (float*)d_out;
 
-  hipLaunchKernelGGL(kS, dim3(2048 + 512 + 1024), dim3(NTH), 0, stream, x, ws);
-  hipLaunchKernelGGL(k4_gate, dim3(BQ), dim3(NTH), 0, stream,
-                     dw7, dw15, dw31, dw63, bn_g, bn_b, bn_m, bn_v,
+  hipLaunchKernelGGL(k1_spec, dim3(1024), dim3(NTH), 0, stream, x, ws);
+  hipLaunchKernelGGL(k2_conv, dim3(1024), dim3(NTH), 0, stream,
+                     x, dw7, dw15, dw31, dw63, bn_g, bn_b, bn_m, bn_v,
                      comp_w1, comp_b1, comp_w2, comp_b2,
                      pn_g, pn_b, pn_m, pn_v, pe_w1, pe_b1, pe_w2, pe_b2,
-                     pg_w, pg_b, temperature, ws);
-  hipLaunchKernelGGL(k5_conv, dim3(BQ * CN), dim3(NTH), 0, stream, x, ws, out);
-  hipLaunchKernelGGL(k6_final, dim3(BQ * 32), dim3(NTH), 0, stream,
+                     pg_w, pg_b, temperature, ws, out);
+  hipLaunchKernelGGL(k3_final, dim3(1024), dim3(NTH), 0, stream,
                      x, proj_w, proj_b, gn_g, gn_b, res_scale, ws, out);
 }
```
